# Kernel tuning notes

Measured on AMD Instinct MI355X. Metric: run time of the kernel, lower is better.

## Reference

```python
import jax, jax.numpy as jnp
import numpy as np

NEG_INF = -1000000.0
B_, NG, HEADS, C, GH, GW, GD = 256, 64, 6, 192, 6, 6, 6
N = GH * GW * GD
POS_DIM = (C // 4) // 4  # DynamicPosBias(dim//4): pos_dim = (dim//4)//4 = 12


def setup_inputs() -> dict:
    key = jax.random.key(0)
    ks = jax.random.split(key, 12)
    rn = lambda k, shape, s=0.02: jax.random.normal(k, shape, jnp.float32) * s
    x = jax.random.normal(ks[0], (B_, N, C), jnp.float32)
    y = jax.random.normal(ks[1], (B_, N, C), jnp.float32)
    # 0 / -1e6 window mask, as produced by the padding logic upstream
    mask = jnp.where(jax.random.bernoulli(ks[2], 0.1, (NG, N, N)), NEG_INF, 0.0).astype(jnp.float32)
    return dict(
        x=x, y=y, mask=mask,
        Wqkv=rn(ks[3], (3 * C, C)), bqkv=jnp.zeros((3 * C,), jnp.float32),
        Wproj=rn(ks[4], (C, C)), bproj=jnp.zeros((C,), jnp.float32),
        pos_proj_w=rn(ks[5], (POS_DIM, 3)), pos_proj_b=jnp.zeros((POS_DIM,), jnp.float32),
        ln1_g=jnp.ones((POS_DIM,), jnp.float32), ln1_b=jnp.zeros((POS_DIM,), jnp.float32),
        pos1_w=rn(ks[6], (POS_DIM, POS_DIM)), pos1_b=jnp.zeros((POS_DIM,), jnp.float32),
        ln2_g=jnp.ones((POS_DIM,), jnp.float32), ln2_b=jnp.zeros((POS_DIM,), jnp.float32),
        pos2_w=rn(ks[7], (POS_DIM, POS_DIM)), pos2_b=jnp.zeros((POS_DIM,), jnp.float32),
        ln3_g=jnp.ones((POS_DIM,), jnp.float32), ln3_b=jnp.zeros((POS_DIM,), jnp.float32),
        pos3_w=rn(ks[8], (HEADS, POS_DIM)), pos3_b=jnp.zeros((HEADS,), jnp.float32),
        H=GH, W=GW, D=GD)


def _ln(t, g, b):
    m = t.mean(-1, keepdims=True)
    v = ((t - m) ** 2).mean(-1, keepdims=True)
    return (t - m) / jnp.sqrt(v + 1e-5) * g + b


def _rel_tables(H, W, D):
    # biases: all relative offsets in [1-H,H-1]x[1-W,W-1]x[1-D,D-1], shape (M, 3)
    ph = np.arange(1 - H, H); pw = np.arange(1 - W, W); pd = np.arange(1 - D, D)
    biases = np.stack(np.meshgrid(ph, pw, pd, indexing='ij')).reshape(3, -1).T.astype(np.float32)
    coords = np.stack(np.meshgrid(np.arange(H), np.arange(W), np.arange(D), indexing='ij')).reshape(3, -1)
    rel = (coords[:, :, None] - coords[:, None, :]).transpose(1, 2, 0)  # (N, N, 3)
    rel[..., 0] += H - 1; rel[..., 1] += W - 1; rel[..., 2] += D - 1
    rel[..., 0] *= (2 * W - 1) * (2 * D - 1); rel[..., 1] *= (2 * D - 1)
    idx = rel.sum(-1)  # (N, N) indices into the (M,) bias table
    return jnp.asarray(biases), jnp.asarray(idx)


def reference(x, y, mask, Wqkv, bqkv, Wproj, bproj, pos_proj_w, pos_proj_b,
              ln1_g, ln1_b, pos1_w, pos1_b, ln2_g, ln2_b, pos2_w, pos2_b,
              ln3_g, ln3_b, pos3_w, pos3_b, H, W, D):
    Bt, n, c = x.shape
    heads = pos3_w.shape[0]
    hd = c // heads
    scale = hd ** (-0.5)
    # NOTE: original code applies self.qkv to BOTH x and y (qkv_y layer unused)
    qkv = (x @ Wqkv.T + bqkv).reshape(Bt, n, 3, heads, hd).transpose(2, 0, 3, 1, 4)
    qkv_y = (y @ Wqkv.T + bqkv).reshape(Bt, n, 3, heads, hd).transpose(2, 0, 3, 1, 4)
    q = qkv[0] * scale
    k_y, v_y = qkv_y[1], qkv_y[2]
    attn = jnp.einsum('bhnd,bhmd->bhnm', q, k_y)
    # dynamic relative position bias: tiny MLP over offsets, then gather
    biases, idx = _rel_tables(H, W, D)
    pos = biases @ pos_proj_w.T + pos_proj_b
    pos = jnp.maximum(_ln(pos, ln1_g, ln1_b), 0) @ pos1_w.T + pos1_b
    pos = jnp.maximum(_ln(pos, ln2_g, ln2_b), 0) @ pos2_w.T + pos2_b
    pos = jnp.maximum(_ln(pos, ln3_g, ln3_b), 0) @ pos3_w.T + pos3_b  # (M, heads)
    rpb = pos[idx.reshape(-1)].reshape(n, n, heads).transpose(2, 0, 1)  # (heads, N, N)
    attn = attn + rpb[None]
    nG = mask.shape[0]
    attn = attn.reshape(Bt // nG, nG, heads, n, n) + mask[None, :, None]
    attn = jax.nn.softmax(attn, axis=-1).reshape(Bt, heads, n, n)
    out = jnp.einsum('bhnm,bhmd->bhnd', attn, v_y).transpose(0, 2, 1, 3).reshape(Bt, n, c)
    return out @ Wproj.T + bproj
```

## Files before the change

### kernel.cpp

```cpp
#include <hip/hip_runtime.h>
#include <stdint.h>

using short8   = __attribute__((ext_vector_type(8))) short;
using float4_  = __attribute__((ext_vector_type(4))) float;
using ushort4_ = __attribute__((ext_vector_type(4))) unsigned short;
typedef unsigned int  uint;
typedef unsigned short ushort;

__device__ __forceinline__ float bf2f(ushort b) {
  uint u = ((uint)b) << 16;
  return __builtin_bit_cast(float, u);
}
__device__ __forceinline__ ushort f2bf(float f) {
  uint u = __builtin_bit_cast(uint, f);
  u = u + 0x7fffu + ((u >> 16) & 1u);
  return (ushort)(u >> 16);
}

#define NN   216
#define NSQ  46656
#define PADV (-3.0e6f)

#define WA_WQKV   0
#define WA_BQKV   110592
#define WA_WPROJ  111168
#define WA_BPROJ  148032
#define WA_PPW    148224
#define WA_PPB    148260
#define WA_G1     148272
#define WA_B1     148284
#define WA_W1     148296
#define WA_WB1    148440
#define WA_G2     148452
#define WA_B2     148464
#define WA_W2     148476
#define WA_WB2    148620
#define WA_G3     148632
#define WA_B3     148644
#define WA_W3     148656
#define WA_WB3    148728
#define WA_TOTAL  148740

__global__ void detect_kernel(const uint* __restrict__ x, int* __restrict__ flag) {
  int lane = threadIdx.x;
  uint w = x[lane];
  ushort lo = (ushort)(w & 0xffffu);
  int e = (lo >> 7) & 0xff;
  int sane = (lo == 0 || (e >= 0x60 && e <= 0x9f)) ? 1 : 0;
  unsigned long long b = __ballot(sane);
  if (lane == 0) flag[0] = (__popcll(b) >= 56) ? 0 : 1;
}

struct SrcPtrs { const void* p[18]; };

__global__ void convert_kernel(SrcPtrs sp, ushort* __restrict__ dst,
                               const int* __restrict__ flag) {
  constexpr int OFF[19] = {WA_WQKV, WA_BQKV, WA_WPROJ, WA_BPROJ, WA_PPW, WA_PPB,
                           WA_G1, WA_B1, WA_W1, WA_WB1, WA_G2, WA_B2, WA_W2,
                           WA_WB2, WA_G3, WA_B3, WA_W3, WA_WB3, WA_TOTAL};
  int t = blockIdx.x * 256 + threadIdx.x;
  if (t >= WA_TOTAL) return;
  int a = 0;
#pragma unroll
  for (int i = 1; i < 18; ++i) a += (t >= OFF[i]) ? 1 : 0;
  int local = t - OFF[a];
  const void* s = sp.p[a];
  ushort v;
  if (flag[0]) v = f2bf(((const float*)s)[local]);
  else         v = ((const ushort*)s)[local];
  dst[t] = v;
}

__global__ __launch_bounds__(256) void cvt_kernel(const float* __restrict__ src,
                                                  ushort* __restrict__ dst,
                                                  const int* __restrict__ flag) {
  if (flag[0] == 0) return;
  size_t s = ((size_t)blockIdx.x * 256 + threadIdx.x) * 8;
  float4_ lo = *(const float4_*)(src + s);
  float4_ hi = *(const float4_*)(src + s + 4);
  short8 pk;
#pragma unroll
  for (int j = 0; j < 4; ++j) {
    pk[j]     = (short)f2bf(lo[j]);
    pk[4 + j] = (short)f2bf(hi[j]);
  }
  *(short8*)(dst + s) = pk;
}

__device__ __forceinline__ void ln_relu(const float* p, const ushort* g,
                                        const ushort* b, float* r) {
  float m = 0.f;
#pragma unroll
  for (int t = 0; t < 12; ++t) m += p[t];
  m *= (1.f / 12.f);
  float v = 0.f;
#pragma unroll
  for (int t = 0; t < 12; ++t) { float d = p[t] - m; v += d * d; }
  v *= (1.f / 12.f);
  float inv = rsqrtf(v + 1e-5f);
#pragma unroll
  for (int t = 0; t < 12; ++t) {
    float z = (p[t] - m) * inv * bf2f(g[t]) + bf2f(b[t]);
    r[t] = fmaxf(z, 0.f);
  }
}

__global__ void pos_mlp_kernel(const ushort* __restrict__ wa, float* __restrict__ pos) {
  int m = blockIdx.x * blockDim.x + threadIdx.x;
  if (m >= 1331) return;
  const ushort* pw  = wa + WA_PPW;  const ushort* pb  = wa + WA_PPB;
  const ushort* g1  = wa + WA_G1;   const ushort* b1  = wa + WA_B1;
  const ushort* w1  = wa + WA_W1;   const ushort* wb1 = wa + WA_WB1;
  const ushort* g2  = wa + WA_G2;   const ushort* b2  = wa + WA_B2;
  const ushort* w2  = wa + WA_W2;   const ushort* wb2 = wa + WA_WB2;
  const ushort* g3  = wa + WA_G3;   const ushort* b3  = wa + WA_B3;
  const ushort* w3  = wa + WA_W3;   const ushort* wb3 = wa + WA_WB3;

  int ih = m / 121, rem = m - ih * 121;
  int iw = rem / 11, id = rem - iw * 11;
  float fh = (float)(ih - 5), fw = (float)(iw - 5), fd = (float)(id - 5);
  float p[12], r[12], q[12];
#pragma unroll
  for (int t = 0; t < 12; ++t)
    p[t] = fh * bf2f(pw[t * 3]) + fw * bf2f(pw[t * 3 + 1]) +
           fd * bf2f(pw[t * 3 + 2]) + bf2f(pb[t]);
  ln_relu(p, g1, b1, r);
#pragma unroll
  for (int t = 0; t < 12; ++t) {
    float s = bf2f(wb1[t]);
#pragma unroll
    for (int u = 0; u < 12; ++u) s += r[u] * bf2f(w1[t * 12 + u]);
    q[t] = s;
  }
  ln_relu(q, g2, b2, r);
#pragma unroll
  for (int t = 0; t < 12; ++t) {
    float s = bf2f(wb2[t]);
#pragma unroll
    for (int u = 0; u < 12; ++u) s += r[u] * bf2f(w2[t * 12 + u]);
    p[t] = s;
  }
  ln_relu(p, g3, b3, r);
#pragma unroll
  for (int h = 0; h < 6; ++h) {
    float s = bf2f(wb3[h]);
#pragma unroll
    for (int u = 0; u < 12; ++u) s += r[u] * bf2f(w3[h * 12 + u]);
    pos[m * 6 + h] = s;
  }
}

__global__ void rpbfrag_kernel(const float* __restrict__ pos, ushort* __restrict__ out) {
  int tgl = blockIdx.x * 256 + threadIdx.x;
  if (tgl >= 6 * 196 * 64) return;
  int lane = tgl & 63;
  int tj   = (tgl >> 6) % 196;
  int h    = (tgl >> 6) / 196;
  int tt = tj / 14, j = tj - tt * 14;
  int l16 = lane & 15, quad = lane >> 4;
  int col = j * 16 + l16;
  int h2 = col / 36, r2 = col - h2 * 36, w2 = r2 / 6, d2 = r2 - w2 * 6;
  ushort4_ o;
#pragma unroll
  for (int r = 0; r < 4; ++r) {
    int i = tt * 16 + quad * 4 + r;
    float val = PADV;
    if (i < 216 && col < 216) {
      int h1 = i / 36, r1 = i - h1 * 36, w1 = r1 / 6, d1 = r1 - w1 * 6;
      int idx = ((h1 - h2 + 5) * 11 + (w1 - w2 + 5)) * 11 + (d1 - d2 + 5);
      val = pos[idx * 6 + h];
    }
    o[r] = f2bf(val);
  }
  *(ushort4_*)(out + (size_t)tgl * 4) = o;
}

__global__ void maskfrag_kernel(const void* __restrict__ maskv,
                                const int* __restrict__ flag,
                                ushort* __restrict__ out) {
  int tgl = blockIdx.x * 256 + threadIdx.x;
  if (tgl >= 64 * 196 * 64) return;
  bool mf32 = flag[0] != 0;
  int lane = tgl & 63;
  int tj   = (tgl >> 6) % 196;
  int g    = (tgl >> 6) / 196;
  int tt = tj / 14, j = tj - tt * 14;
  int l16 = lane & 15, quad = lane >> 4;
  int col = j * 16 + l16;
  const float*  mf = (const float*)maskv + (size_t)g * NSQ;
  const ushort* mu = (const ushort*)maskv + (size_t)g * NSQ;
  ushort4_ o;
#pragma unroll
  for (int r = 0; r < 4; ++r) {
    int i = tt * 16 + quad * 4 + r;
    float val = PADV;
    if (i < 216 && col < 216) {
      int mi = i * 216 + col;
      val = mf32 ? mf[mi] : bf2f(mu[mi]);
    }
    o[r] = f2bf(val);
  }
  *(ushort4_*)(out + (size_t)tgl * 4) = o;
}

__global__ __launch_bounds__(256) void gemm_kernel(
    const void* __restrict__ p0,
    const ushort* __restrict__ p1,
    const void* __restrict__ p2,
    const ushort* __restrict__ W,  const ushort* __restrict__ bias,
    void* __restrict__ dq, void* __restrict__ dk, void* __restrict__ dv,
    const int* __restrict__ flag, int is_proj) {
  __shared__ __align__(16) ushort b_lds[2304 * 8];

  int tid = threadIdx.x;
  int m0 = blockIdx.x * 128;
  int n0 = blockIdx.y * 96;
  int z  = blockIdx.z;
  int wbase = is_proj ? 0 : z * 192;
  float scale = (!is_proj && z == 0) ? 0.17677669529663687f : 1.0f;
  void* dst = (z == 0) ? dq : (z == 1 ? dk : dv);
  int fl = flag[0];
  bool f32path = (!is_proj) && (z == 0) && (fl != 0);
  bool o_f32 = is_proj && (fl != 0);

  const ushort* A16;
  if (is_proj)      A16 = p1;
  else if (z == 0)  A16 = (const ushort*)p0;
  else              A16 = fl ? p1 : (const ushort*)p2;
  const float* A32 = (const float*)p0;

  int lane = tid & 63, w = tid >> 6;
  int l16 = lane & 15, quad = lane >> 4;

  for (int s = tid; s < 2304; s += 256) {
    int kk = s / 384;
    int rem = s - kk * 384;
    int nt = rem >> 6;
    int l  = rem & 63;
    int l16v = l & 15, qv = l >> 4;
    short8 pk = *(const short8*)(W + (size_t)(wbase + n0 + nt * 16 + l16v) * 192 + kk * 32 + qv * 8);
    *(short8*)(b_lds + s * 8) = pk;
  }
  __syncthreads();

  float4_ acc[2][6];
#pragma unroll
  for (int mt = 0; mt < 2; ++mt)
#pragma unroll
    for (int nt = 0; nt < 6; ++nt) acc[mt][nt] = (float4_){0.f, 0.f, 0.f, 0.f};

#pragma unroll
  for (int kk = 0; kk < 6; ++kk) {
    short8 af[2];
#pragma unroll
    for (int mt = 0; mt < 2; ++mt) {
      size_t abase = (size_t)(m0 + w * 32 + mt * 16 + l16) * 192 + kk * 32 + quad * 8;
      if (f32path) {
        float4_ lo = *(const float4_*)(A32 + abase);
        float4_ hi = *(const float4_*)(A32 + abase + 4);
#pragma unroll
        for (int j = 0; j < 4; ++j) {
          af[mt][j]     = (short)f2bf(lo[j]);
          af[mt][4 + j] = (short)f2bf(hi[j]);
        }
      } else {
        af[mt] = *(const short8*)(A16 + abase);
      }
    }
    short8 bfr[6];
#pragma unroll
    for (int nt = 0; nt < 6; ++nt)
      bfr[nt] = *(const short8*)(b_lds + ((kk * 6 + nt) * 64 + lane) * 8);
#pragma unroll
    for (int mt = 0; mt < 2; ++mt)
#pragma unroll
      for (int nt = 0; nt < 6; ++nt)
        acc[mt][nt] = __builtin_amdgcn_mfma_f32_16x16x32_bf16(af[mt], bfr[nt], acc[mt][nt], 0, 0, 0);
  }

#pragma unroll
  for (int mt = 0; mt < 2; ++mt) {
#pragma unroll
    for (int nt = 0; nt < 6; ++nt) {
      int lcol = n0 + nt * 16 + l16;
      float bv = bf2f(bias[(is_proj ? 0 : z * 192) + lcol]);
#pragma unroll
      for (int r = 0; r < 4; ++r) {
        int grow = m0 + w * 32 + mt * 16 + quad * 4 + r;
        float val = (acc[mt][nt][r] + bv) * scale;
        if (is_proj) {
          if (o_f32) ((float*)dst)[(size_t)grow * 192 + lcol] = val;
          else       ((ushort*)dst)[(size_t)grow * 192 + lcol] = f2bf(val);
        } else {
          int bb = grow / 216;
          int nn2 = grow - bb * 216;
          int hh = lcol >> 5, dd = lcol & 31;
          ((ushort*)dst)[(((size_t)bb * 6 + hh) * 216 + nn2) * 32 + dd] = f2bf(val);
        }
      }
    }
  }
}

__global__ __launch_bounds__(256) void attn_kernel(
    const ushort* __restrict__ q, const ushort* __restrict__ k,
    const ushort* __restrict__ v, const ushort* __restrict__ rpbf,
    const ushort* __restrict__ maskf, ushort* __restrict__ opre) {
  __shared__ __align__(16) ushort vts[32 * 232];
  __shared__ __align__(16) ushort ps[4][16 * 232];

  int bid = blockIdx.x;
  int b = bid / 6, h = bid - b * 6;
  int g = b & 63;
  int tid = threadIdx.x, lane = tid & 63, w = tid >> 6;
  int l16 = lane & 15, quad = lane >> 4;

  const ushort* qh = q + (size_t)(b * 6 + h) * 6912;
  const ushort* kh = k + (size_t)(b * 6 + h) * 6912;
  const ushort* vh = v + (size_t)(b * 6 + h) * 6912;

  for (int i = tid; i < (32 * 232) / 2; i += 256) ((uint*)vts)[i] = 0u;
  __syncthreads();
  for (int i = tid; i < 864; i += 256) {
    int n = i >> 2, dp = (i & 3) * 8;
    uint4 raw = *(const uint4*)(vh + n * 32 + dp);
    const ushort* ep = reinterpret_cast<const ushort*>(&raw);
#pragma unroll
    for (int jj = 0; jj < 8; ++jj) vts[(dp + jj) * 232 + n] = ep[jj];
  }
  __syncthreads();

  for (int t = w; t < 14; t += 4) {
    int r0 = t * 16;
    const ushort* rf = rpbf  + ((size_t)(h * 196 + t * 14) * 64 + lane) * 4;
    const ushort* mf = maskf + ((size_t)(g * 196 + t * 14) * 64 + lane) * 4;
    short8 aq = *(const short8*)(qh + (r0 + l16) * 32 + quad * 8);

    float4_ s[14];
#pragma unroll
    for (int j = 0; j < 14; ++j) {
      ushort4_ rb = *(const ushort4_*)(rf + j * 256);
      ushort4_ mb = *(const ushort4_*)(mf + j * 256);
      float4_ cin;
#pragma unroll
      for (int r = 0; r < 4; ++r) cin[r] = bf2f(rb[r]) + bf2f(mb[r]);
      short8 bk = *(const short8*)(kh + (j * 16 + l16) * 32 + quad * 8);
      s[j] = __builtin_amdgcn_mfma_f32_16x16x32_bf16(aq, bk, cin, 0, 0, 0);
    }

#pragma unroll
    for (int r = 0; r < 4; ++r) {
      float mx = -1e30f;
#pragma unroll
      for (int j = 0; j < 14; ++j) mx = fmaxf(mx, s[j][r]);
      mx = fmaxf(mx, __shfl_xor(mx, 1));
      mx = fmaxf(mx, __shfl_xor(mx, 2));
      mx = fmaxf(mx, __shfl_xor(mx, 4));
      mx = fmaxf(mx, __shfl_xor(mx, 8));
      float sum = 0.f;
#pragma unroll
      for (int j = 0; j < 14; ++j) {
        float pe = __expf(s[j][r] - mx);
        s[j][r] = pe;
        sum += pe;
      }
      sum += __shfl_xor(sum, 1);
      sum += __shfl_xor(sum, 2);
      sum += __shfl_xor(sum, 4);
      sum += __shfl_xor(sum, 8);
      float inv = 1.0f / sum;
#pragma unroll
      for (int j = 0; j < 14; ++j)
        ps[w][(quad * 4 + r) * 232 + j * 16 + l16] = f2bf(s[j][r] * inv);
    }

    asm volatile("s_waitcnt lgkmcnt(0)" ::: "memory");

    float4_ o0 = (float4_){0.f, 0.f, 0.f, 0.f};
    float4_ o1 = (float4_){0.f, 0.f, 0.f, 0.f};
#pragma unroll
    for (int kt = 0; kt < 7; ++kt) {
      short8 pf = *(const short8*)(&ps[w][l16 * 232 + kt * 32 + quad * 8]);
      short8 v0 = *(const short8*)(&vts[(l16) * 232 + kt * 32 + quad * 8]);
      short8 v1 = *(const short8*)(&vts[(16 + l16) * 232 + kt * 32 + quad * 8]);
      o0 = __builtin_amdgcn_mfma_f32_16x16x32_bf16(pf, v0, o0, 0, 0, 0);
      o1 = __builtin_amdgcn_mfma_f32_16x16x32_bf16(pf, v1, o1, 0, 0, 0);
    }

#pragma unroll
    for (int r = 0; r < 4; ++r) {
      int i = r0 + quad * 4 + r;
      if (i < 216) {
        size_t base = ((size_t)b * 216 + i) * 192 + h * 32;
        opre[base + l16]      = f2bf(o0[r]);
        opre[base + 16 + l16] = f2bf(o1[r]);
      }
    }
  }
}

extern "C" void kernel_launch(void* const* d_in, const int* in_sizes, int n_in,
                              void* d_out, int out_size, void* d_ws, size_t ws_size,
                              hipStream_t stream) {
  (void)in_sizes; (void)n_in; (void)out_size; (void)ws_size;

  char* p = (char*)d_ws;
  int*    flag   = (int*)p;            p += 256;
  ushort* warena = (ushort*)p;         p += 298240;
  float*  pos    = (float*)p;          p += 32768;
  ushort* rpbf   = (ushort*)p;         p += 602112;
  ushort* maskf  = (ushort*)p;         p += 6422528;
  ushort* ycvt   = (ushort*)p;         p += 21234688;
  ushort* qb     = (ushort*)p;         p += 21234688;
  ushort* kb     = (ushort*)p;         p += 21234688;
  ushort* vb     = (ushort*)p;
  ushort* opre   = ycvt;

  detect_kernel<<<1, 64, 0, stream>>>((const uint*)d_in[0], flag);

  SrcPtrs sp;
  for (int i = 0; i < 18; ++i) sp.p[i] = d_in[3 + i];
  convert_kernel<<<(WA_TOTAL + 255) / 256, 256, 0, stream>>>(sp, warena, flag);

  cvt_kernel<<<5184, 256, 0, stream>>>((const float*)d_in[1], ycvt, flag);

  pos_mlp_kernel<<<6, 256, 0, stream>>>(warena, pos);
  rpbfrag_kernel<<<294, 256, 0, stream>>>(pos, rpbf);
  maskfrag_kernel<<<3136, 256, 0, stream>>>(d_in[2], flag, maskf);

  gemm_kernel<<<dim3(432, 2, 3), 256, 0, stream>>>(
      d_in[0], ycvt, d_in[1], warena + WA_WQKV, warena + WA_BQKV,
      qb, kb, vb, flag, 0);

  attn_kernel<<<1536, 256, 0, stream>>>(qb, kb, vb, rpbf, maskf, opre);

  gemm_kernel<<<dim3(432, 2, 1), 256, 0, stream>>>(
      opre, opre, opre, warena + WA_WPROJ, warena + WA_BPROJ,
      d_out, d_out, d_out, flag, 1);
}
```

Baseline: 322.0 us.

## Keep softmax probabilities in registers via transposed QK^T and pre-fragmented V

The attention kernel now computes S^T (K as A operand), so each lane holds a full column of scores for one query row. That lets the row max and sum reduce over lanes with only two shuffles, and lets probabilities feed the PV MFMA straight from registers (16x16x16 bf16) instead of round-tripping through LDS. V is staged into LDS already laid out as MFMA B-fragments, and normalization is deferred to the output store. The rpb and mask fragment kernels are changed to the transposed layout, with vectorized mask loads. The cost is more MFMA instructions of smaller K-depth, plus an uncoalesced scalar gather when building the V fragments.

```diff
diff --git a/kernel.cpp b/kernel.cpp
--- a/kernel.cpp
+++ b/kernel.cpp
@@ -2,6 +2,7 @@
 #include <stdint.h>
 
 using short8   = __attribute__((ext_vector_type(8))) short;
+using short4_  = __attribute__((ext_vector_type(4))) short;
 using float4_  = __attribute__((ext_vector_type(4))) float;
 using ushort4_ = __attribute__((ext_vector_type(4))) unsigned short;
 typedef unsigned int  uint;
@@ -20,6 +21,16 @@
 #define NN   216
 #define NSQ  46656
 #define PADV (-3.0e6f)
+
+#if __has_builtin(__builtin_amdgcn_mfma_f32_16x16x16bf16_1k)
+  #define HAVE_MFMA16 1
+  #define MFMA16(a, b, c) __builtin_amdgcn_mfma_f32_16x16x16bf16_1k(a, b, c, 0, 0, 0)
+#elif __has_builtin(__builtin_amdgcn_mfma_f32_16x16x16_bf16)
+  #define HAVE_MFMA16 1
+  #define MFMA16(a, b, c) __builtin_amdgcn_mfma_f32_16x16x16_bf16(a, b, c, 0, 0, 0)
+#else
+  #define HAVE_MFMA16 0
+#endif
 
 #define WA_WQKV   0
 #define WA_BQKV   110592
@@ -156,21 +167,23 @@
   int lane = tgl & 63;
   int tj   = (tgl >> 6) % 196;
   int h    = (tgl >> 6) / 196;
-  int tt = tj / 14, j = tj - tt * 14;
+  int tt = tj / 14, jt = tj - tt * 14;
   int l16 = lane & 15, quad = lane >> 4;
-  int col = j * 16 + l16;
-  int h2 = col / 36, r2 = col - h2 * 36, w2 = r2 / 6, d2 = r2 - w2 * 6;
+  int i = tt * 16 + l16;
+  int jbase = jt * 16 + quad * 4;
   ushort4_ o;
-#pragma unroll
-  for (int r = 0; r < 4; ++r) {
-    int i = tt * 16 + quad * 4 + r;
-    float val = PADV;
-    if (i < 216 && col < 216) {
-      int h1 = i / 36, r1 = i - h1 * 36, w1 = r1 / 6, d1 = r1 - w1 * 6;
+  if (i < 216 && jbase < 216) {
+    int h1 = i / 36, r1 = i - h1 * 36, w1 = r1 / 6, d1 = r1 - w1 * 6;
+#pragma unroll
+    for (int r = 0; r < 4; ++r) {
+      int j = jbase + r;
+      int h2 = j / 36, r2 = j - h2 * 36, w2 = r2 / 6, d2 = r2 - w2 * 6;
       int idx = ((h1 - h2 + 5) * 11 + (w1 - w2 + 5)) * 11 + (d1 - d2 + 5);
-      val = pos[idx * 6 + h];
-    }
-    o[r] = f2bf(val);
+      o[r] = f2bf(pos[idx * 6 + h]);
+    }
+  } else {
+#pragma unroll
+    for (int r = 0; r < 4; ++r) o[r] = f2bf(PADV);
   }
   *(ushort4_*)(out + (size_t)tgl * 4) = o;
 }
@@ -184,21 +197,23 @@
   int lane = tgl & 63;
   int tj   = (tgl >> 6) % 196;
   int g    = (tgl >> 6) / 196;
-  int tt = tj / 14, j = tj - tt * 14;
+  int tt = tj / 14, jt = tj - tt * 14;
   int l16 = lane & 15, quad = lane >> 4;
-  int col = j * 16 + l16;
-  const float*  mf = (const float*)maskv + (size_t)g * NSQ;
-  const ushort* mu = (const ushort*)maskv + (size_t)g * NSQ;
+  int i = tt * 16 + l16;
+  int jbase = jt * 16 + quad * 4;
   ushort4_ o;
-#pragma unroll
-  for (int r = 0; r < 4; ++r) {
-    int i = tt * 16 + quad * 4 + r;
-    float val = PADV;
-    if (i < 216 && col < 216) {
-      int mi = i * 216 + col;
-      val = mf32 ? mf[mi] : bf2f(mu[mi]);
-    }
-    o[r] = f2bf(val);
+  if (i < 216 && jbase < 216) {
+    int mi = i * 216 + jbase;
+    if (mf32) {
+      float4_ mv = *(const float4_*)((const float*)maskv + (size_t)g * NSQ + mi);
+#pragma unroll
+      for (int r = 0; r < 4; ++r) o[r] = f2bf(mv[r]);
+    } else {
+      o = *(const ushort4_*)((const ushort*)maskv + (size_t)g * NSQ + mi);
+    }
+  } else {
+#pragma unroll
+    for (int r = 0; r < 4; ++r) o[r] = f2bf(PADV);
   }
   *(ushort4_*)(out + (size_t)tgl * 4) = o;
 }
@@ -306,8 +321,11 @@
     const ushort* __restrict__ q, const ushort* __restrict__ k,
     const ushort* __restrict__ v, const ushort* __restrict__ rpbf,
     const ushort* __restrict__ maskf, ushort* __restrict__ opre) {
-  __shared__ __align__(16) ushort vts[32 * 232];
-  __shared__ __align__(16) ushort ps[4][16 * 232];
+#if HAVE_MFMA16
+  __shared__ __align__(16) ushort vfrag[28 * 64 * 4];
+#else
+  __shared__ __align__(16) ushort vfrag[14 * 64 * 8];
+#endif
 
   int bid = blockIdx.x;
   int b = bid / 6, h = bid - b * 6;
@@ -319,15 +337,29 @@
   const ushort* kh = k + (size_t)(b * 6 + h) * 6912;
   const ushort* vh = v + (size_t)(b * 6 + h) * 6912;
 
-  for (int i = tid; i < (32 * 232) / 2; i += 256) ((uint*)vts)[i] = 0u;
-  __syncthreads();
-  for (int i = tid; i < 864; i += 256) {
-    int n = i >> 2, dp = (i & 3) * 8;
-    uint4 raw = *(const uint4*)(vh + n * 32 + dp);
-    const ushort* ep = reinterpret_cast<const ushort*>(&raw);
-#pragma unroll
-    for (int jj = 0; jj < 8; ++jj) vts[(dp + jj) * 232 + n] = ep[jj];
-  }
+#if HAVE_MFMA16
+  for (int pos = tid; pos < 1792; pos += 256) {
+    int chunk = pos >> 6, l = pos & 63;
+    int kt = chunk >> 1, dh = chunk & 1;
+    int qd = l >> 4, lv = l & 15;
+    ushort4_ tmp;
+#pragma unroll
+    for (int j = 0; j < 4; ++j)
+      tmp[j] = vh[(kt * 16 + qd * 4 + j) * 32 + dh * 16 + lv];
+    *(ushort4_*)(vfrag + pos * 4) = tmp;
+  }
+#else
+  for (int pos = tid; pos < 896; pos += 256) {
+    int chunk = pos >> 6, l = pos & 63;
+    int kt2 = chunk >> 1, dh = chunk & 1;
+    int qd = l >> 4, lv = l & 15;
+    short8 tmp;
+#pragma unroll
+    for (int j = 0; j < 8; ++j)
+      tmp[j] = (short)vh[(kt2 * 32 + qd * 8 + j) * 32 + dh * 16 + lv];
+    *(short8*)(vfrag + pos * 8) = tmp;
+  }
+#endif
   __syncthreads();
 
   for (int t = w; t < 14; t += 4) {
@@ -336,64 +368,84 @@
     const ushort* mf = maskf + ((size_t)(g * 196 + t * 14) * 64 + lane) * 4;
     short8 aq = *(const short8*)(qh + (r0 + l16) * 32 + quad * 8);
 
-    float4_ s[14];
-#pragma unroll
-    for (int j = 0; j < 14; ++j) {
-      ushort4_ rb = *(const ushort4_*)(rf + j * 256);
-      ushort4_ mb = *(const ushort4_*)(mf + j * 256);
+    float4_ st[14];
+#pragma unroll
+    for (int jt = 0; jt < 14; ++jt) {
+      ushort4_ rb = *(const ushort4_*)(rf + jt * 256);
+      ushort4_ mb = *(const ushort4_*)(mf + jt * 256);
       float4_ cin;
 #pragma unroll
       for (int r = 0; r < 4; ++r) cin[r] = bf2f(rb[r]) + bf2f(mb[r]);
-      short8 bk = *(const short8*)(kh + (j * 16 + l16) * 32 + quad * 8);
-      s[j] = __builtin_amdgcn_mfma_f32_16x16x32_bf16(aq, bk, cin, 0, 0, 0);
-    }
-
-#pragma unroll
-    for (int r = 0; r < 4; ++r) {
-      float mx = -1e30f;
-#pragma unroll
-      for (int j = 0; j < 14; ++j) mx = fmaxf(mx, s[j][r]);
-      mx = fmaxf(mx, __shfl_xor(mx, 1));
-      mx = fmaxf(mx, __shfl_xor(mx, 2));
-      mx = fmaxf(mx, __shfl_xor(mx, 4));
-      mx = fmaxf(mx, __shfl_xor(mx, 8));
-      float sum = 0.f;
-#pragma unroll
-      for (int j = 0; j < 14; ++j) {
-        float pe = __expf(s[j][r] - mx);
-        s[j][r] = pe;
+      short8 bk = *(const short8*)(kh + (jt * 16 + l16) * 32 + quad * 8);
+      st[jt] = __builtin_amdgcn_mfma_f32_16x16x32_bf16(bk, aq, cin, 0, 0, 0);
+    }
+
+    float mx = -1e30f;
+#pragma unroll
+    for (int jt = 0; jt < 14; ++jt)
+#pragma unroll
+      for (int r = 0; r < 4; ++r) mx = fmaxf(mx, st[jt][r]);
+    mx = fmaxf(mx, __shfl_xor(mx, 16));
+    mx = fmaxf(mx, __shfl_xor(mx, 32));
+    float sum = 0.f;
+#pragma unroll
+    for (int jt = 0; jt < 14; ++jt)
+#pragma unroll
+      for (int r = 0; r < 4; ++r) {
+        float pe = __expf(st[jt][r] - mx);
+        st[jt][r] = pe;
         sum += pe;
       }
-      sum += __shfl_xor(sum, 1);
-      sum += __shfl_xor(sum, 2);
-      sum += __shfl_xor(sum, 4);
-      sum += __shfl_xor(sum, 8);
-      float inv = 1.0f / sum;
-#pragma unroll
-      for (int j = 0; j < 14; ++j)
-        ps[w][(quad * 4 + r) * 232 + j * 16 + l16] = f2bf(s[j][r] * inv);
-    }
-
-    asm volatile("s_waitcnt lgkmcnt(0)" ::: "memory");
+    sum += __shfl_xor(sum, 16);
+    sum += __shfl_xor(sum, 32);
+    float inv = 1.0f / sum;
 
     float4_ o0 = (float4_){0.f, 0.f, 0.f, 0.f};
     float4_ o1 = (float4_){0.f, 0.f, 0.f, 0.f};
-#pragma unroll
-    for (int kt = 0; kt < 7; ++kt) {
-      short8 pf = *(const short8*)(&ps[w][l16 * 232 + kt * 32 + quad * 8]);
-      short8 v0 = *(const short8*)(&vts[(l16) * 232 + kt * 32 + quad * 8]);
-      short8 v1 = *(const short8*)(&vts[(16 + l16) * 232 + kt * 32 + quad * 8]);
-      o0 = __builtin_amdgcn_mfma_f32_16x16x32_bf16(pf, v0, o0, 0, 0, 0);
-      o1 = __builtin_amdgcn_mfma_f32_16x16x32_bf16(pf, v1, o1, 0, 0, 0);
-    }
+
+#if HAVE_MFMA16
+#pragma unroll
+    for (int kt = 0; kt < 14; ++kt) {
+      short4_ pa;
+#pragma unroll
+      for (int r = 0; r < 4; ++r) pa[r] = (short)f2bf(st[kt][r]);
+      short4_ vb0 = *(const short4_*)(vfrag + ((kt * 2 + 0) * 64 + lane) * 4);
+      short4_ vb1 = *(const short4_*)(vfrag + ((kt * 2 + 1) * 64 + lane) * 4);
+      o0 = MFMA16(pa, vb0, o0);
+      o1 = MFMA16(pa, vb1, o1);
+    }
+#else
+#pragma unroll
+    for (int kt2 = 0; kt2 < 7; ++kt2) {
+      uint pe0 = ((uint)f2bf(st[2*kt2][0])) | (((uint)f2bf(st[2*kt2][1])) << 16);
+      uint pe1 = ((uint)f2bf(st[2*kt2][2])) | (((uint)f2bf(st[2*kt2][3])) << 16);
+      uint po0 = ((uint)f2bf(st[2*kt2+1][0])) | (((uint)f2bf(st[2*kt2+1][1])) << 16);
+      uint po1 = ((uint)f2bf(st[2*kt2+1][2])) | (((uint)f2bf(st[2*kt2+1][3])) << 16);
+      int slo = (((2 * quad) & 3) << 4) | l16;
+      int shi = (((2 * quad + 1) & 3) << 4) | l16;
+      uint e_lo0 = __shfl((int)pe0, slo), e_lo1 = __shfl((int)pe1, slo);
+      uint o_lo0 = __shfl((int)po0, slo), o_lo1 = __shfl((int)po1, slo);
+      uint e_hi0 = __shfl((int)pe0, shi), e_hi1 = __shfl((int)pe1, shi);
+      uint o_hi0 = __shfl((int)po0, shi), o_hi1 = __shfl((int)po1, shi);
+      uint lo0 = (quad < 2) ? e_lo0 : o_lo0, lo1 = (quad < 2) ? e_lo1 : o_lo1;
+      uint hi0 = (quad < 2) ? e_hi0 : o_hi0, hi1 = (quad < 2) ? e_hi1 : o_hi1;
+      uint4 paw = {lo0, lo1, hi0, hi1};
+      short8 pa = __builtin_bit_cast(short8, paw);
+      short8 vb0 = *(const short8*)(vfrag + ((kt2 * 2 + 0) * 64 + lane) * 8);
+      short8 vb1 = *(const short8*)(vfrag + ((kt2 * 2 + 1) * 64 + lane) * 8);
+      o0 = __builtin_amdgcn_mfma_f32_16x16x32_bf16(pa, vb0, o0, 0, 0, 0);
+      o1 = __builtin_amdgcn_mfma_f32_16x16x32_bf16(pa, vb1, o1, 0, 0, 0);
+    }
+#endif
 
 #pragma unroll
     for (int r = 0; r < 4; ++r) {
+      float ir = __shfl(inv, quad * 4 + r);
       int i = r0 + quad * 4 + r;
       if (i < 216) {
         size_t base = ((size_t)b * 216 + i) * 192 + h * 32;
-        opre[base + l16]      = f2bf(o0[r]);
-        opre[base + 16 + l16] = f2bf(o1[r]);
+        opre[base + l16]      = f2bf(o0[r] * ir);
+        opre[base + 16 + l16] = f2bf(o1[r] * ir);
       }
     }
   }
```

Result: faster. 303.3 us (-5.8%).
